# Kernel optimization log

Measured on AMD Instinct MI355X. Metric: run time of the kernel, lower is better.

Reference implementation:

```python
import jax, jax.numpy as jnp
import numpy as np

N = 50000        # nodes
E = 600000       # edges (before self-loops)
IN_DIM = 128
HID = 128
EMB = 128
DEC = 64
B = 1024         # drug pairs
NEG_GAT = 0.2    # GATConv leaky-relu slope
NEG_DEC = 0.1    # decoder LeakyReLU slope
EPS = 1e-5       # BatchNorm eps


def setup_inputs() -> dict:
    key = jax.random.key(0)
    ks = jax.random.split(key, 16)
    rn = lambda k, s, sc=0.05: jax.random.normal(k, s, dtype=jnp.float32) * sc
    return dict(
        x=rn(ks[0], (N, IN_DIM), 1.0),
        edge_index=jax.random.randint(ks[1], (2, E), 0, N, dtype=jnp.int32),
        drug_index=jax.random.randint(ks[2], (B, 2), 1, N + 1, dtype=jnp.int32),
        W1=rn(ks[3], (HID, IN_DIM)), att1=rn(ks[4], (1, 1, 2 * HID)), b1=jnp.zeros((HID,), jnp.float32),
        g1=jnp.ones((HID,), jnp.float32), be1=jnp.zeros((HID,), jnp.float32),
        W2=rn(ks[5], (HID, HID)), att2=rn(ks[6], (1, 1, 2 * HID)), b2=jnp.zeros((HID,), jnp.float32),
        g2=jnp.ones((HID,), jnp.float32), be2=jnp.zeros((HID,), jnp.float32),
        W3=rn(ks[7], (EMB, HID)), att3=rn(ks[8], (1, 1, 2 * EMB)), b3=jnp.zeros((EMB,), jnp.float32),
        g3=jnp.ones((EMB,), jnp.float32), be3=jnp.zeros((EMB,), jnp.float32),
        P1=rn(ks[9], (EMB, DEC), 0.1), P2=rn(ks[10], (DEC, DEC), 0.1),
    )


def _segment_softmax(alpha, seg, n):
    amax = jax.ops.segment_max(alpha, seg, num_segments=n)
    amax = jnp.where(jnp.isfinite(amax), amax, 0.0)
    ex = jnp.exp(alpha - amax[seg])
    den = jax.ops.segment_sum(ex, seg, num_segments=n)
    return ex / (den[seg] + 1e-16)


def _gat(x, src, dst, W, att, b):
    # num_head == 1 (required by original att-parameter shape)
    n = x.shape[0]
    d = W.shape[0]
    h = (x @ W.T)[:, None, :]                    # [N,1,d]
    x_i, x_j = h[dst], h[src]                    # target, source per edge
    # alpha = (cat([x_i,x_j],-1)*att).sum(-1) without materializing the concat
    alpha = (x_i * att[..., :d]).sum(-1) + (x_j * att[..., d:]).sum(-1)  # [E,1]
    alpha = jax.nn.leaky_relu(alpha, NEG_GAT)
    # NOTE: original code softmaxes over edge_index[0] (src) while aggregating by dst
    alpha = _segment_softmax(alpha, src, n)
    out = jax.ops.segment_sum(x_j * alpha[:, :, None], dst, num_segments=n)
    return jax.nn.relu(out.reshape(n, -1) + b)


def _bn(x, g, b):
    # BatchNorm1d (training-mode batch statistics, biased var)
    mu = x.mean(0)
    var = x.var(0)
    return (x - mu) * jax.lax.rsqrt(var + EPS) * g + b


def reference(x, edge_index, drug_index, W1, att1, b1, g1, be1,
              W2, att2, b2, g2, be2, W3, att3, b3, g3, be3, P1, P2):
    n = x.shape[0]
    loops = jnp.arange(n, dtype=edge_index.dtype)
    src = jnp.concatenate([edge_index[0], loops])  # add_self_loops
    dst = jnp.concatenate([edge_index[1], loops])
    h = jax.nn.leaky_relu(_bn(_gat(x, src, dst, W1, att1, b1), g1, be1), NEG_DEC)
    h = jax.nn.leaky_relu(_bn(_gat(h, src, dst, W2, att2, b2), g2, be2), NEG_DEC)
    h = jax.nn.leaky_relu(_bn(_gat(h, src, dst, W3, att3, b3), g3, be3), NEG_DEC)
    a = h[drug_index[:, 0] - 1]                    # [B,EMB]
    bvec = h[drug_index[:, 1] - 1]                 # [B,EMB]
    M = P1 @ P2 @ P1.T                             # [EMB,EMB] bilinear form
    ypred = jnp.einsum('bd,de,be->b', a, M, bvec)[:, None]  # [B,1]
    return ypred
```

## Files before the change

kernel.cpp:

```cpp
#include <hip/hip_runtime.h>
#include <hip/hip_bf16.h>

#define DEVINL __device__ __forceinline__

constexpr int N  = 50000;
constexpr int E  = 600000;
constexpr int TE = E + N;
constexpr int D  = 128;
constexpr int GEMM_ROWS = 128;
constexpr int GEMM_B = (N + GEMM_ROWS - 1) / GEMM_ROWS;
constexpr int HST_STRIDE = 136;

constexpr int NBUCK = (N + 255) >> 8;
constexpr int NSB   = 2 * NBUCK;
constexpr int CHUNK = 2560;
constexpr int EB3   = (TE + CHUNK - 1) / CHUNK;
constexpr int EB3P  = 256;

constexpr int FUSE_CNT = EB3;
constexpr int FUSE_WB  = FUSE_CNT + 192;

typedef short bf16x8 __attribute__((ext_vector_type(8)));
typedef float f32x4  __attribute__((ext_vector_type(4)));

DEVINL float lrelu(float x, float s) { return x >= 0.f ? x : s * x; }

DEVINL unsigned short f2bf(float f) {
    unsigned u = __float_as_uint(f);
    u += 0x7FFFu + ((u >> 16) & 1u);
    return (unsigned short)(u >> 16);
}
DEVINL float bfl(unsigned u) { return __uint_as_float(u << 16); }
DEVINL float bfh(unsigned u) { return __uint_as_float(u & 0xFFFF0000u); }

DEVINL void edge_sd(int e, const int* ei, int& s, int& d) {
    if (e < E) { s = ei[e]; d = ei[E + e]; }
    else       { s = d = e - E; }
}

__global__ __launch_bounds__(256) void k_fused0(const int* __restrict__ ei,
                                                unsigned* __restrict__ hist,
                                                const float* __restrict__ W0,
                                                const float* __restrict__ W1,
                                                const float* __restrict__ W2,
                                                unsigned short* __restrict__ Wb) {
    __shared__ unsigned cnt[NSB];
    int b = blockIdx.x;
    if (b < FUSE_CNT) {
        for (int t = threadIdx.x; t < NSB; t += 256) cnt[t] = 0;
        __syncthreads();
        int base = b * CHUNK;
        for (int i = threadIdx.x; i < CHUNK; i += 256) {
            int e = base + i;
            if (e < TE) {
                int s, d; edge_sd(e, ei, s, d);
                atomicAdd(&cnt[d >> 8], 1u);
                atomicAdd(&cnt[NBUCK + (s >> 8)], 1u);
            }
        }
        __syncthreads();
        unsigned* row = hist + (size_t)b * NSB;
        for (int t = threadIdx.x; t < NSB; t += 256) row[t] = cnt[t];
    } else {
        int bb = b - FUSE_CNT;
        int l = bb >> 6;
        const float* W = (l == 0) ? W0 : (l == 1) ? W1 : W2;
        int t = (bb & 63) * 256 + threadIdx.x;
        Wb[l * 16384 + t] = f2bf(W[t]);
    }
}

__global__ __launch_bounds__(256) void k_gemm(const float* __restrict__ X,
                                              const unsigned short* __restrict__ O16,
                                              const unsigned short* __restrict__ Wb,
                                              unsigned short* __restrict__ Hb16,
                                              const float* __restrict__ att,
                                              float* __restrict__ ai,
                                              float* __restrict__ ajx,
                                              const float* __restrict__ csum,
                                              const float* __restrict__ csq,
                                              const float* __restrict__ g,
                                              const float* __restrict__ be,
                                              int apply_bn) {
    __shared__ unsigned short hst[4][32][HST_STRIDE];
    __shared__ float ssl[256];
    int wave = threadIdx.x >> 6, lane = threadIdx.x & 63;
    int m = lane & 15, quad = lane >> 4;
    int r0 = blockIdx.x * GEMM_ROWS + wave * 32;

    if (apply_bn) {
        if (threadIdx.x < 128) {
            int c = threadIdx.x;
            float mean = csum[c] / (float)N;
            float var  = csq[c] / (float)N - mean * mean;
            float scale = g[c] * rsqrtf(var + 1e-5f);
            ssl[c] = scale;
            ssl[128 + c] = be[c] - mean * scale;
        }
        __syncthreads();
    }

    bf16x8 afrag[2][4];
    #pragma unroll
    for (int tile = 0; tile < 2; tile++) {
        int rowA = r0 + tile * 16 + m;
        bool rowok = rowA < N;
        #pragma unroll
        for (int k4 = 0; k4 < 4; k4++) {
            int c0 = k4 * 32 + quad * 8;
            float v[8];
            if (rowok) {
                if (apply_bn) {
                    uint4 hu = *(const uint4*)(O16 + (size_t)rowA * D + c0);
                    v[0] = bfl(hu.x); v[1] = bfh(hu.x);
                    v[2] = bfl(hu.y); v[3] = bfh(hu.y);
                    v[4] = bfl(hu.z); v[5] = bfh(hu.z);
                    v[6] = bfl(hu.w); v[7] = bfh(hu.w);
                    #pragma unroll
                    for (int j = 0; j < 8; j++)
                        v[j] = lrelu(v[j] * ssl[c0 + j] + ssl[128 + c0 + j], 0.1f);
                } else {
                    float4 x0 = *(const float4*)(X + (size_t)rowA * D + c0);
                    float4 x1 = *(const float4*)(X + (size_t)rowA * D + c0 + 4);
                    v[0] = x0.x; v[1] = x0.y; v[2] = x0.z; v[3] = x0.w;
                    v[4] = x1.x; v[5] = x1.y; v[6] = x1.z; v[7] = x1.w;
                }
            } else {
                #pragma unroll
                for (int j = 0; j < 8; j++) v[j] = 0.f;
            }
            #pragma unroll
            for (int j = 0; j < 8; j++) afrag[tile][k4][j] = (short)f2bf(v[j]);
        }
    }

    float pii[2][4] = {{0.f,0.f,0.f,0.f},{0.f,0.f,0.f,0.f}};
    float pjj[2][4] = {{0.f,0.f,0.f,0.f},{0.f,0.f,0.f,0.f}};
    #pragma unroll
    for (int nt = 0; nt < 8; nt++) {
        int n0 = nt * 16;
        f32x4 acc0 = {0.f, 0.f, 0.f, 0.f};
        f32x4 acc1 = {0.f, 0.f, 0.f, 0.f};
        const unsigned short* wrow = Wb + (size_t)(n0 + m) * D + quad * 8;
        #pragma unroll
        for (int k4 = 0; k4 < 4; k4++) {
            bf16x8 bfr = *(const bf16x8*)(wrow + k4 * 32);
            acc0 = __builtin_amdgcn_mfma_f32_16x16x32_bf16(afrag[0][k4], bfr, acc0, 0, 0, 0);
            acc1 = __builtin_amdgcn_mfma_f32_16x16x32_bf16(afrag[1][k4], bfr, acc1, 0, 0, 0);
        }
        float ad = att[n0 + m];
        float as = att[128 + n0 + m];
        #pragma unroll
        for (int i = 0; i < 4; i++) {
            hst[wave][quad * 4 + i][n0 + m]      = f2bf(acc0[i]);
            hst[wave][16 + quad * 4 + i][n0 + m] = f2bf(acc1[i]);
            pii[0][i] += acc0[i] * ad;
            pjj[0][i] += acc0[i] * as;
            pii[1][i] += acc1[i] * ad;
            pjj[1][i] += acc1[i] * as;
        }
    }

    #pragma unroll
    for (int t = 0; t < 8; t++) {
        int r = t * 4 + quad;
        int row = r0 + r;
        int cb = m * 8;
        uint4 vv = *(const uint4*)&hst[wave][r][cb];
        if (row < N)
            *(uint4*)(Hb16 + (size_t)row * D + cb) = vv;
    }

    #pragma unroll
    for (int mask = 8; mask >= 1; mask >>= 1) {
        #pragma unroll
        for (int tile = 0; tile < 2; tile++) {
            #pragma unroll
            for (int i = 0; i < 4; i++) {
                pii[tile][i] += __shfl_xor(pii[tile][i], mask);
                pjj[tile][i] += __shfl_xor(pjj[tile][i], mask);
            }
        }
    }
    if (m == 0) {
        #pragma unroll
        for (int tile = 0; tile < 2; tile++) {
            #pragma unroll
            for (int i = 0; i < 4; i++) {
                int row = r0 + tile * 16 + quad * 4 + i;
                if (row < N) { ai[row] = pii[tile][i]; ajx[2 * (size_t)row] = pjj[tile][i]; }
            }
        }
    }
}

__global__ __launch_bounds__(256) void k_bscan(const unsigned* __restrict__ hist,
                                               unsigned* __restrict__ pref,
                                               unsigned* __restrict__ btot,
                                               const float* __restrict__ P1,
                                               const float* __restrict__ P2,
                                               float* __restrict__ Mm) {
    __shared__ unsigned sc[256];
    __shared__ float trow[128];
    int sb = blockIdx.x, t = threadIdx.x;
    if (sb >= NSB) {
        int bb = sb - NSB;
        if (t < 128) {
            int i = bb * 2 + (t >> 6), d = t & 63;
            float s = 0.f;
            #pragma unroll 8
            for (int k = 0; k < 64; k++) s += P1[i * 64 + k] * P2[k * 64 + d];
            trow[t] = s;
        }
        __syncthreads();
        int tg = bb * 256 + t;
        int j = tg & 127;
        const float* Tr = trow + (t >> 7) * 64;
        float s = 0.f;
        #pragma unroll 8
        for (int d = 0; d < 64; d++) s += Tr[d] * P1[j * 64 + d];
        Mm[tg] = s;
        return;
    }
    unsigned v = (t < EB3) ? hist[(size_t)t * NSB + sb] : 0;
    sc[t] = v;
    __syncthreads();
    #pragma unroll
    for (int off = 1; off < 256; off <<= 1) {
        unsigned add = (t >= off) ? sc[t - off] : 0;
        __syncthreads();
        sc[t] += add;
        __syncthreads();
    }
    if (t < EB3) pref[(size_t)sb * EB3P + t] = sc[t] - v;
    if (t == EB3 - 1) btot[sb] = sc[t];
}

__global__ __launch_bounds__(256) void k_boff(const unsigned* __restrict__ btot,
                                              unsigned* __restrict__ boff2,
                                              int* __restrict__ ptrbase) {
    __shared__ unsigned sc[256];
    int t = threadIdx.x;
    for (int side = 0; side < 2; side++) {
        unsigned v = (t < NBUCK) ? btot[side * NBUCK + t] : 0;
        sc[t] = v;
        __syncthreads();
        #pragma unroll
        for (int off = 1; off < 256; off <<= 1) {
            unsigned add = (t >= off) ? sc[t - off] : 0;
            __syncthreads();
            sc[t] += add;
            __syncthreads();
        }
        if (t < NBUCK) boff2[side * (NBUCK + 1) + t] = sc[t] - v;
        if (t == NBUCK - 1) boff2[side * (NBUCK + 1) + NBUCK] = sc[t];
        __syncthreads();
    }
    if (t == 0) { ptrbase[N] = TE; ptrbase[(N + 8) + N] = TE; }
}

__global__ __launch_bounds__(256) void k_scatter(const int* __restrict__ ei,
                                                 const unsigned* __restrict__ pref,
                                                 const unsigned* __restrict__ boff2,
                                                 unsigned* __restrict__ sorted) {
    __shared__ unsigned alloc[NSB];
    int j = blockIdx.x;
    for (int t = threadIdx.x; t < NSB; t += 256) {
        int side = t >= NBUCK;
        int bucket = t - side * NBUCK;
        alloc[t] = boff2[side * (NBUCK + 1) + bucket] + pref[(size_t)t * EB3P + j]
                 + (side ? (unsigned)TE : 0u);
    }
    __syncthreads();
    int base = j * CHUNK;
    for (int i = threadIdx.x; i < CHUNK; i += 256) {
        int e = base + i;
        if (e < TE) {
            int s, d; edge_sd(e, ei, s, d);
            unsigned pd = atomicAdd(&alloc[d >> 8], 1u);
            sorted[pd] = ((unsigned)(d & 255) << 16) | (unsigned)s;
            unsigned ps = atomicAdd(&alloc[NBUCK + (s >> 8)], 1u);
            sorted[ps] = ((unsigned)(s & 255) << 16) | (unsigned)d;
        }
    }
}

__global__ __launch_bounds__(256) void k_csr(const unsigned* __restrict__ sorted,
                                             const unsigned* __restrict__ boff2,
                                             int* __restrict__ ptrbase,
                                             unsigned short* __restrict__ srcc,
                                             unsigned short* __restrict__ dstc) {
    __shared__ unsigned cnt[256];
    __shared__ unsigned sc[256];
    int sb = blockIdx.x, t = threadIdx.x;
    int side = sb >= NBUCK;
    int bucket = sb - side * NBUCK;
    unsigned beg = boff2[side * (NBUCK + 1) + bucket];
    unsigned end = boff2[side * (NBUCK + 1) + bucket + 1];
    const unsigned* srt = sorted + (side ? (size_t)TE : 0);
    unsigned short* out = side ? dstc : srcc;
    int* ptr = ptrbase + (size_t)side * (N + 8);
    cnt[t] = 0;
    __syncthreads();
    for (unsigned idx = beg + t; idx < end; idx += 256)
        atomicAdd(&cnt[srt[idx] >> 16], 1u);
    __syncthreads();
    unsigned own = cnt[t];
    sc[t] = own;
    __syncthreads();
    #pragma unroll
    for (int off = 1; off < 256; off <<= 1) {
        unsigned add = (t >= off) ? sc[t - off] : 0;
        __syncthreads();
        sc[t] += add;
        __syncthreads();
    }
    unsigned loc = sc[t] - own;
    int v = (bucket << 8) + t;
    if (v < N) ptr[v] = (int)(beg + loc);
    cnt[t] = beg + loc;
    __syncthreads();
    for (unsigned idx = beg + t; idx < end; idx += 256) {
        unsigned u = srt[idx];
        unsigned pos = atomicAdd(&cnt[u >> 16], 1u);
        out[pos] = (unsigned short)u;
    }
}

__global__ __launch_bounds__(256) void k_den(const int* __restrict__ srcp,
                                             const unsigned short* __restrict__ dstc,
                                             const float* __restrict__ ai,
                                             float* __restrict__ ajx,
                                             float* __restrict__ csumz) {
    if (blockIdx.x == 0) csumz[threadIdx.x] = 0.f;
    int g = threadIdx.x >> 4, l16 = threadIdx.x & 15;
    int v = blockIdx.x * 16 + g;
    if (v >= N) return;
    int beg = srcp[v], end = srcp[v + 1];
    float ajv = ajx[2 * (size_t)v];
    float acc = 0.f;
    for (int idx = beg + l16; idx < end; idx += 16) {
        int d = dstc[idx];
        acc += __expf(lrelu(ai[d] + ajv, 0.2f));
    }
    #pragma unroll
    for (int mask = 8; mask >= 1; mask >>= 1) acc += __shfl_xor(acc, mask);
    if (l16 == 0) ajx[2 * (size_t)v + 1] = 1.0f / (acc + 1e-16f);
}

__global__ __launch_bounds__(256) void k_aggregate(const int* __restrict__ rowp,
                                                   const unsigned short* __restrict__ srcc,
                                                   const float* __restrict__ ai,
                                                   const float2* __restrict__ ajinv,
                                                   const uint2* __restrict__ Hu2,
                                                   const float* __restrict__ bvec,
                                                   unsigned short* __restrict__ O16) {
    int wid = threadIdx.x >> 6, lane = threadIdx.x & 63;
    int h = lane >> 5, l32 = lane & 31;
    int v = blockIdx.x * 4 + wid;
    if (v >= N) return;
    int beg = rowp[v], end = rowp[v + 1];
    float aiv = ai[v];
    float a0 = 0.f, a1 = 0.f, a2 = 0.f, a3 = 0.f;
    int idx = beg;
    for (; idx + 8 <= end; idx += 8) {
        int    s[4];
        float2 aw[4];
        uint2  u[4];
        #pragma unroll
        for (int t = 0; t < 4; t++) s[t] = srcc[idx + 2 * t + h];
        #pragma unroll
        for (int t = 0; t < 4; t++) aw[t] = ajinv[s[t]];
        #pragma unroll
        for (int t = 0; t < 4; t++) u[t] = Hu2[(size_t)s[t] * 32 + l32];
        #pragma unroll
        for (int t = 0; t < 4; t++) {
            float w = __expf(lrelu(aiv + aw[t].x, 0.2f)) * aw[t].y;
            a0 += w * bfl(u[t].x);
            a1 += w * bfh(u[t].x);
            a2 += w * bfl(u[t].y);
            a3 += w * bfh(u[t].y);
        }
    }
    int R = end - idx;
    if (R > 0) {
        int    s[4];
        float2 aw[4];
        uint2  u[4];
        #pragma unroll
        for (int t = 0; t < 4; t++) {
            int sl = idx + 2 * t + h;
            s[t] = srcc[sl < end ? sl : beg];
        }
        #pragma unroll
        for (int t = 0; t < 4; t++) aw[t] = ajinv[s[t]];
        #pragma unroll
        for (int t = 0; t < 4; t++) u[t] = Hu2[(size_t)s[t] * 32 + l32];
        #pragma unroll
        for (int t = 0; t < 4; t++) {
            float w = (2 * t + h < R) ? __expf(lrelu(aiv + aw[t].x, 0.2f)) * aw[t].y : 0.f;
            a0 += w * bfl(u[t].x);
            a1 += w * bfh(u[t].x);
            a2 += w * bfl(u[t].y);
            a3 += w * bfh(u[t].y);
        }
    }
    a0 += __shfl_xor(a0, 32);
    a1 += __shfl_xor(a1, 32);
    a2 += __shfl_xor(a2, 32);
    a3 += __shfl_xor(a3, 32);
    if (h == 0) {
        float4 b = ((const float4*)bvec)[l32];
        float o0 = fmaxf(a0 + b.x, 0.f);
        float o1 = fmaxf(a1 + b.y, 0.f);
        float o2 = fmaxf(a2 + b.z, 0.f);
        float o3 = fmaxf(a3 + b.w, 0.f);
        uint2 st;
        st.x = (unsigned)f2bf(o0) | ((unsigned)f2bf(o1) << 16);
        st.y = (unsigned)f2bf(o2) | ((unsigned)f2bf(o3) << 16);
        *(uint2*)(O16 + (size_t)v * D + l32 * 4) = st;
    }
}

__global__ __launch_bounds__(256) void k_stats(const unsigned short* __restrict__ O16,
                                               float* __restrict__ colsum, float* __restrict__ colsq) {
    int c4 = (threadIdx.x & 31) * 4;
    int rg = threadIdx.x >> 5;
    float s0=0.f,s1=0.f,s2=0.f,s3=0.f,q0=0.f,q1=0.f,q2=0.f,q3=0.f;
    for (int v = blockIdx.x * 8 + rg; v < N; v += gridDim.x * 8) {
        uint2 u = *(const uint2*)(O16 + (size_t)v * D + c4);
        float v0 = bfl(u.x), v1 = bfh(u.x), v2 = bfl(u.y), v3 = bfh(u.y);
        s0 += v0; q0 += v0 * v0;
        s1 += v1; q1 += v1 * v1;
        s2 += v2; q2 += v2 * v2;
        s3 += v3; q3 += v3 * v3;
    }
    __shared__ float ls[8][128], lq[8][128];
    ls[rg][c4+0]=s0; ls[rg][c4+1]=s1; ls[rg][c4+2]=s2; ls[rg][c4+3]=s3;
    lq[rg][c4+0]=q0; lq[rg][c4+1]=q1; lq[rg][c4+2]=q2; lq[rg][c4+3]=q3;
    __syncthreads();
    if (threadIdx.x < 128) {
        int c = threadIdx.x;
        float s = 0.f, q = 0.f;
        #pragma unroll
        for (int r = 0; r < 8; r++) { s += ls[r][c]; q += lq[r][c]; }
        atomicAdd(colsum + c, s);
        atomicAdd(colsq + c, q);
    }
}

__global__ __launch_bounds__(128) void k_pred(const unsigned short* __restrict__ O16,
                                              const float* __restrict__ csum,
                                              const float* __restrict__ csq,
                                              const float* __restrict__ g,
                                              const float* __restrict__ be,
                                              const int* __restrict__ drug,
                                              const float* __restrict__ M,
                                              float* __restrict__ out) {
    int b = blockIdx.x, i = threadIdx.x;
    __shared__ float av[128], bv[128];
    int ia = drug[b * 2] - 1, ib = drug[b * 2 + 1] - 1;
    float mean = csum[i] / (float)N;
    float var  = csq[i] / (float)N - mean * mean;
    float scale = g[i] * rsqrtf(var + 1e-5f);
    float shift = be[i] - mean * scale;
    float ha = __uint_as_float(((unsigned)O16[(size_t)ia * D + i]) << 16);
    float hb = __uint_as_float(((unsigned)O16[(size_t)ib * D + i]) << 16);
    av[i] = lrelu(ha * scale + shift, 0.1f);
    bv[i] = lrelu(hb * scale + shift, 0.1f);
    __syncthreads();
    const float4* M4  = (const float4*)(M + (size_t)i * 128);
    const float4* bv4 = (const float4*)bv;
    float u = 0.f;
    #pragma unroll 8
    for (int j = 0; j < 32; j++) {
        float4 mv = M4[j];
        float4 bb = bv4[j];
        u += mv.x * bb.x + mv.y * bb.y + mv.z * bb.z + mv.w * bb.w;
    }
    float val = av[i] * u;
    #pragma unroll
    for (int off = 32; off; off >>= 1) val += __shfl_down(val, off);
    __shared__ float red[2];
    if ((i & 63) == 0) red[i >> 6] = val;
    __syncthreads();
    if (i == 0) out[b] = red[0] + red[1];
}

extern "C" void kernel_launch(void* const* d_in, const int* in_sizes, int n_in,
                              void* d_out, int out_size, void* d_ws, size_t ws_size,
                              hipStream_t stream) {
    const float* x    = (const float*)d_in[0];
    const int*   ei   = (const int*)  d_in[1];
    const int*   drug = (const int*)  d_in[2];
    const float* W[3]   = {(const float*)d_in[3], (const float*)d_in[8],  (const float*)d_in[13]};
    const float* att[3] = {(const float*)d_in[4], (const float*)d_in[9],  (const float*)d_in[14]};
    const float* bb[3]  = {(const float*)d_in[5], (const float*)d_in[10], (const float*)d_in[15]};
    const float* gg[3]  = {(const float*)d_in[6], (const float*)d_in[11], (const float*)d_in[16]};
    const float* be[3]  = {(const float*)d_in[7], (const float*)d_in[12], (const float*)d_in[17]};
    const float* P1 = (const float*)d_in[18];
    const float* P2 = (const float*)d_in[19];

    float* ws = (float*)d_ws;
    size_t o_H      = 0;
    size_t o_O      = o_H + (size_t)N * 64;
    size_t o_ai     = o_O + (size_t)N * 64;
    size_t o_ajinv  = o_ai + N;
    size_t o_colsum = o_ajinv + 2 * (size_t)N;
    size_t o_colsq  = o_colsum + 128;
    size_t o_hist   = o_colsq + 128;
    size_t o_pref   = o_hist + (size_t)EB3 * NSB;
    size_t o_btot   = o_pref + (size_t)NSB * EB3P;
    size_t o_boff2  = o_btot + 512;
    size_t o_sorted = o_boff2 + 512;
    size_t o_rowptr = o_sorted + 2 * (size_t)TE;
    size_t o_srcp   = o_rowptr + N + 8;
    size_t o_src    = o_srcp + N + 8;
    size_t o_dstc   = o_src + TE / 2 + 8;
    size_t o_Mm     = o_dstc + TE / 2 + 8;
    size_t o_Wb     = o_Mm + 128 * 128;

    unsigned short* Hb16 = (unsigned short*)(ws + o_H);
    uint2*          Hu2  = (uint2*)(ws + o_H);
    unsigned short* O16  = (unsigned short*)(ws + o_O);
    float*    ai    = ws + o_ai;
    float*    ajx   = ws + o_ajinv;
    float2*   ajinv = (float2*)(ws + o_ajinv);
    float*    csum  = ws + o_colsum;
    float*    csq   = ws + o_colsq;
    unsigned* hist  = (unsigned*)(ws + o_hist);
    unsigned* pref  = (unsigned*)(ws + o_pref);
    unsigned* btot  = (unsigned*)(ws + o_btot);
    unsigned* boff2 = (unsigned*)(ws + o_boff2);
    unsigned* sorted= (unsigned*)(ws + o_sorted);
    int*      rowp  = (int*)(ws + o_rowptr);
    int*      srcp  = (int*)(ws + o_srcp);
    unsigned short* srcc = (unsigned short*)(ws + o_src);
    unsigned short* dstc = (unsigned short*)(ws + o_dstc);
    float*    Mm    = ws + o_Mm;
    unsigned short* Wb = (unsigned short*)(ws + o_Wb);

    const int NB4  = (N + 3) / 4;
    const int NB16 = (N + 15) / 16;

    k_fused0<<<FUSE_WB, 256, 0, stream>>>(ei, hist, W[0], W[1], W[2], Wb);

    k_bscan  <<<NSB + 64, 256, 0, stream>>>(hist, pref, btot, P1, P2, Mm);
    k_boff   <<<1,   256, 0, stream>>>(btot, boff2, rowp);
    k_scatter<<<EB3, 256, 0, stream>>>(ei, pref, boff2, sorted);
    k_csr    <<<NSB, 256, 0, stream>>>(sorted, boff2, rowp, srcc, dstc);

    for (int l = 0; l < 3; l++) {
        k_gemm<<<GEMM_B, 256, 0, stream>>>(x, O16, Wb + l * 16384, Hb16, att[l],
                                           ai, ajx, csum, csq, gg[l == 0 ? 0 : l - 1],
                                           be[l == 0 ? 0 : l - 1], l > 0 ? 1 : 0);
        k_den<<<NB16, 256, 0, stream>>>(srcp, dstc, ai, ajx, csum);
        k_aggregate<<<NB4, 256, 0, stream>>>(rowp, srcc, ai, ajinv, Hu2, bb[l], O16);
        k_stats<<<256, 256, 0, stream>>>(O16, csum, csq);
    }

    k_pred<<<1024, 128, 0, stream>>>(O16, csum, csq, gg[2], be[2], drug, Mm, (float*)d_out);
}
```

Measured before the change: 363.3 us.

## Fold bucket-scan kernels into scatter and CSR by recomputing prefixes per block

Removes the separate k_bscan and k_boff launches. Each scatter block now sums the histogram column itself to get its own prefix and the bucket totals, then scans the bucket offsets locally, and each CSR block recomputes its bucket begin and end the same way. This cuts two kernel launches and their global round-trips, but every block redundantly reads the full histogram (EB3×NSB entries) and performs a block scan.

```diff
diff --git a/kernel.cpp b/kernel.cpp
--- a/kernel.cpp
+++ b/kernel.cpp
@@ -15,7 +15,6 @@
 constexpr int NSB   = 2 * NBUCK;
 constexpr int CHUNK = 2560;
 constexpr int EB3   = (TE + CHUNK - 1) / CHUNK;
-constexpr int EB3P  = 256;
 
 constexpr int FUSE_CNT = EB3;
 constexpr int FUSE_WB  = FUSE_CNT + 192;
@@ -194,17 +193,21 @@
     }
 }
 
-__global__ __launch_bounds__(256) void k_bscan(const unsigned* __restrict__ hist,
-                                               unsigned* __restrict__ pref,
-                                               unsigned* __restrict__ btot,
-                                               const float* __restrict__ P1,
-                                               const float* __restrict__ P2,
-                                               float* __restrict__ Mm) {
+__global__ __launch_bounds__(256) void k_scatter(const int* __restrict__ ei,
+                                                 const unsigned* __restrict__ hist,
+                                                 unsigned* __restrict__ sorted,
+                                                 const float* __restrict__ P1,
+                                                 const float* __restrict__ P2,
+                                                 float* __restrict__ Mm) {
+    __shared__ unsigned pref[NSB];
+    __shared__ unsigned tot[NSB];
+    __shared__ unsigned bbase[NSB];
     __shared__ unsigned sc[256];
+    __shared__ unsigned alloc[NSB];
     __shared__ float trow[128];
-    int sb = blockIdx.x, t = threadIdx.x;
-    if (sb >= NSB) {
-        int bb = sb - NSB;
+    int j = blockIdx.x, t = threadIdx.x;
+    if (j >= EB3) {
+        int bb = j - EB3;
         if (t < 128) {
             int i = bb * 2 + (t >> 6), d = t & 63;
             float s = 0.f;
@@ -214,35 +217,27 @@
         }
         __syncthreads();
         int tg = bb * 256 + t;
-        int j = tg & 127;
+        int jj = tg & 127;
         const float* Tr = trow + (t >> 7) * 64;
         float s = 0.f;
         #pragma unroll 8
-        for (int d = 0; d < 64; d++) s += Tr[d] * P1[j * 64 + d];
+        for (int d = 0; d < 64; d++) s += Tr[d] * P1[jj * 64 + d];
         Mm[tg] = s;
         return;
     }
-    unsigned v = (t < EB3) ? hist[(size_t)t * NSB + sb] : 0;
-    sc[t] = v;
-    __syncthreads();
-    #pragma unroll
-    for (int off = 1; off < 256; off <<= 1) {
-        unsigned add = (t >= off) ? sc[t - off] : 0;
-        __syncthreads();
-        sc[t] += add;
-        __syncthreads();
-    }
-    if (t < EB3) pref[(size_t)sb * EB3P + t] = sc[t] - v;
-    if (t == EB3 - 1) btot[sb] = sc[t];
-}
-
-__global__ __launch_bounds__(256) void k_boff(const unsigned* __restrict__ btot,
-                                              unsigned* __restrict__ boff2,
-                                              int* __restrict__ ptrbase) {
-    __shared__ unsigned sc[256];
-    int t = threadIdx.x;
+    unsigned p0 = 0, p1 = 0, T0 = 0, T1 = 0;
+    for (int i = 0; i < EB3; i++) {
+        const unsigned* row = hist + (size_t)i * NSB;
+        unsigned a = row[t];
+        unsigned b = (t + 256 < NSB) ? row[t + 256] : 0;
+        T0 += a; T1 += b;
+        if (i < j) { p0 += a; p1 += b; }
+    }
+    pref[t] = p0; tot[t] = T0;
+    if (t + 256 < NSB) { pref[t + 256] = p1; tot[t + 256] = T1; }
+    __syncthreads();
     for (int side = 0; side < 2; side++) {
-        unsigned v = (t < NBUCK) ? btot[side * NBUCK + t] : 0;
+        unsigned v = (t < NBUCK) ? tot[side * NBUCK + t] : 0;
         sc[t] = v;
         __syncthreads();
         #pragma unroll
@@ -252,24 +247,12 @@
             sc[t] += add;
             __syncthreads();
         }
-        if (t < NBUCK) boff2[side * (NBUCK + 1) + t] = sc[t] - v;
-        if (t == NBUCK - 1) boff2[side * (NBUCK + 1) + NBUCK] = sc[t];
-        __syncthreads();
-    }
-    if (t == 0) { ptrbase[N] = TE; ptrbase[(N + 8) + N] = TE; }
-}
-
-__global__ __launch_bounds__(256) void k_scatter(const int* __restrict__ ei,
-                                                 const unsigned* __restrict__ pref,
-                                                 const unsigned* __restrict__ boff2,
-                                                 unsigned* __restrict__ sorted) {
-    __shared__ unsigned alloc[NSB];
-    int j = blockIdx.x;
-    for (int t = threadIdx.x; t < NSB; t += 256) {
-        int side = t >= NBUCK;
-        int bucket = t - side * NBUCK;
-        alloc[t] = boff2[side * (NBUCK + 1) + bucket] + pref[(size_t)t * EB3P + j]
-                 + (side ? (unsigned)TE : 0u);
+        if (t < NBUCK) bbase[side * NBUCK + t] = sc[t] - v;
+        __syncthreads();
+    }
+    for (int sbt = t; sbt < NSB; sbt += 256) {
+        int side = sbt >= NBUCK;
+        alloc[sbt] = bbase[sbt] + pref[sbt] + (side ? (unsigned)TE : 0u);
     }
     __syncthreads();
     int base = j * CHUNK;
@@ -285,18 +268,40 @@
     }
 }
 
-__global__ __launch_bounds__(256) void k_csr(const unsigned* __restrict__ sorted,
-                                             const unsigned* __restrict__ boff2,
+__global__ __launch_bounds__(256) void k_csr(const unsigned* __restrict__ hist,
+                                             const unsigned* __restrict__ sorted,
                                              int* __restrict__ ptrbase,
                                              unsigned short* __restrict__ srcc,
                                              unsigned short* __restrict__ dstc) {
+    __shared__ unsigned tot[NSB];
+    __shared__ unsigned sc[256];
     __shared__ unsigned cnt[256];
-    __shared__ unsigned sc[256];
+    __shared__ unsigned begend[2];
     int sb = blockIdx.x, t = threadIdx.x;
     int side = sb >= NBUCK;
     int bucket = sb - side * NBUCK;
-    unsigned beg = boff2[side * (NBUCK + 1) + bucket];
-    unsigned end = boff2[side * (NBUCK + 1) + bucket + 1];
+    unsigned T0 = 0, T1 = 0;
+    for (int i = 0; i < EB3; i++) {
+        const unsigned* row = hist + (size_t)i * NSB;
+        T0 += row[t];
+        T1 += (t + 256 < NSB) ? row[t + 256] : 0;
+    }
+    tot[t] = T0;
+    if (t + 256 < NSB) tot[t + 256] = T1;
+    __syncthreads();
+    unsigned v = (t < NBUCK) ? tot[side * NBUCK + t] : 0;
+    sc[t] = v;
+    __syncthreads();
+    #pragma unroll
+    for (int off = 1; off < 256; off <<= 1) {
+        unsigned add = (t >= off) ? sc[t - off] : 0;
+        __syncthreads();
+        sc[t] += add;
+        __syncthreads();
+    }
+    if (t == bucket) { begend[0] = sc[t] - v; begend[1] = sc[t]; }
+    __syncthreads();
+    unsigned beg = begend[0], end = begend[1];
     const unsigned* srt = sorted + (side ? (size_t)TE : 0);
     unsigned short* out = side ? dstc : srcc;
     int* ptr = ptrbase + (size_t)side * (N + 8);
@@ -316,8 +321,9 @@
         __syncthreads();
     }
     unsigned loc = sc[t] - own;
-    int v = (bucket << 8) + t;
-    if (v < N) ptr[v] = (int)(beg + loc);
+    int v2 = (bucket << 8) + t;
+    if (v2 < N) ptr[v2] = (int)(beg + loc);
+    if (t == 0 && bucket == 0) ptr[N] = TE;
     cnt[t] = beg + loc;
     __syncthreads();
     for (unsigned idx = beg + t; idx < end; idx += 256) {
@@ -509,10 +515,7 @@
     size_t o_colsum = o_ajinv + 2 * (size_t)N;
     size_t o_colsq  = o_colsum + 128;
     size_t o_hist   = o_colsq + 128;
-    size_t o_pref   = o_hist + (size_t)EB3 * NSB;
-    size_t o_btot   = o_pref + (size_t)NSB * EB3P;
-    size_t o_boff2  = o_btot + 512;
-    size_t o_sorted = o_boff2 + 512;
+    size_t o_sorted = o_hist + (size_t)EB3 * NSB;
     size_t o_rowptr = o_sorted + 2 * (size_t)TE;
     size_t o_srcp   = o_rowptr + N + 8;
     size_t o_src    = o_srcp + N + 8;
@@ -529,9 +532,6 @@
     float*    csum  = ws + o_colsum;
     float*    csq   = ws + o_colsq;
     unsigned* hist  = (unsigned*)(ws + o_hist);
-    unsigned* pref  = (unsigned*)(ws + o_pref);
-    unsigned* btot  = (unsigned*)(ws + o_btot);
-    unsigned* boff2 = (unsigned*)(ws + o_boff2);
     unsigned* sorted= (unsigned*)(ws + o_sorted);
     int*      rowp  = (int*)(ws + o_rowptr);
     int*      srcp  = (int*)(ws + o_srcp);
@@ -545,10 +545,8 @@
 
     k_fused0<<<FUSE_WB, 256, 0, stream>>>(ei, hist, W[0], W[1], W[2], Wb);
 
-    k_bscan  <<<NSB + 64, 256, 0, stream>>>(hist, pref, btot, P1, P2, Mm);
-    k_boff   <<<1,   256, 0, stream>>>(btot, boff2, rowp);
-    k_scatter<<<EB3, 256, 0, stream>>>(ei, pref, boff2, sorted);
-    k_csr    <<<NSB, 256, 0, stream>>>(sorted, boff2, rowp, srcc, dstc);
+    k_scatter<<<EB3 + 64, 256, 0, stream>>>(ei, hist, sorted, P1, P2, Mm);
+    k_csr    <<<NSB, 256, 0, stream>>>(hist, sorted, rowp, srcc, dstc);
 
     for (int l = 0; l < 3; l++) {
         k_gemm<<<GEMM_B, 256, 0, stream>>>(x, O16, Wb + l * 16384, Hb16, att[l],
```

Measured after the change: 412.9 us. +13.6%, slower.
